# Kernel tuning notes

Measured on AMD Instinct MI355X. Metric: run time of the kernel, lower is better.

The kernel has to match this reference:

```python
import jax, jax.numpy as jnp
import numpy as np

NEG = 0.01  # leaky relu negative_slope
N = 4096    # neurons in this (relu) layer == rows of prev linear W
M = 4096    # inputs to prev linear layer


def setup_inputs() -> dict:
    key = jax.random.key(0)
    k1, k2, k3, k4, k5, k6, k7 = jax.random.split(key, 7)
    center = jax.random.normal(k1, (N,), dtype=jnp.float32)
    radius = jax.random.uniform(k2, (N,), dtype=jnp.float32)
    lowerBound = center - radius
    upperBound = center + radius
    alpha = jax.random.uniform(k3, (N,), minval=NEG, maxval=1.0, dtype=jnp.float32)
    W = jax.random.normal(k4, (N, M), dtype=jnp.float32) / np.float32(np.sqrt(M))
    b = jax.random.normal(k5, (N,), dtype=jnp.float32) * 0.1
    c0 = jax.random.normal(k6, (M,), dtype=jnp.float32)
    r0 = jax.random.uniform(k7, (M,), dtype=jnp.float32)
    return dict(lowerBound=lowerBound, upperBound=upperBound, alpha=alpha,
                W=W, b=b, l0=c0 - r0, u0=c0 + r0)


def reference(lowerBound, upperBound, alpha, W, b, l0, u0):
    ns = jnp.float32(NEG)
    # per-neuron slope/bias bounds (elementwise, exactly as the torch code)
    lw = jnp.full_like(lowerBound, ns)
    uw = jnp.full_like(upperBound, ns)
    ub_bias = jnp.zeros_like(upperBound)
    lb_bias = jnp.zeros_like(lowerBound)
    positive = lowerBound > 0
    lw = jnp.where(positive, 1.0, lw)
    uw = jnp.where(positive, 1.0, uw)
    crossing = (lowerBound < 0) & (upperBound > 0)
    slope = jnp.where(crossing,
                      (upperBound - ns * lowerBound) / (upperBound - lowerBound),
                      0.0)
    uw = jnp.where(crossing, slope, uw)
    ub_bias = jnp.where(crossing, (ns - slope) * lowerBound, ub_bias)
    a = jnp.clip(alpha, ns, 1.0)  # alpha.data.clamp_
    lw = jnp.where(crossing, a, lw)

    # faithful: materialize dense diagonal relational weight matrices [N,N]
    D_l = jnp.diag(lw)
    D_u = jnp.diag(uw)

    # prev (linear) backsubstitution: sign-split + four matmuls + bias accumulation
    Dup, Dun = jnp.maximum(D_u, 0.0), jnp.minimum(D_u, 0.0)
    Dlp, Dln = jnp.maximum(D_l, 0.0), jnp.minimum(D_l, 0.0)
    ub_bias = ub_bias + Dup @ b + Dun @ b   # linear layer: upper bias == lower bias == b
    lb_bias = lb_bias + Dlp @ b + Dln @ b
    Wu = Dup @ W + Dun @ W                  # [N,M]
    Wl = Dlp @ W + Dln @ W

    # input-layer concretization against the input box [l0, u0]
    upper = jnp.maximum(Wu, 0.0) @ u0 + jnp.minimum(Wu, 0.0) @ l0 + ub_bias
    lower = jnp.maximum(Wl, 0.0) @ l0 + jnp.minimum(Wl, 0.0) @ u0 + lb_bias
    return jnp.stack([lower, upper])  # [2, N]
```

## Files before the change

### kernel.cpp

```cpp
#include <hip/hip_runtime.h>

#define NN 4096
#define MM 4096
#define NEG 0.01f

__global__ __launch_bounds__(256, 4) void abstract_leaky_relu_kernel(
    const float* __restrict__ lbnd,
    const float* __restrict__ ubnd,
    const float* __restrict__ alpha,
    const float* __restrict__ W,
    const float* __restrict__ b,
    const float* __restrict__ l0,
    const float* __restrict__ u0,
    float* __restrict__ out)
{
    __shared__ float s_c[MM];
    __shared__ float s_r[MM];

    for (int j = threadIdx.x * 4; j < MM; j += 256 * 4) {
        const float4 l = *(const float4*)(l0 + j);
        const float4 u = *(const float4*)(u0 + j);
        *(float4*)(s_c + j) = make_float4(0.5f*(l.x+u.x), 0.5f*(l.y+u.y),
                                          0.5f*(l.z+u.z), 0.5f*(l.w+u.w));
        *(float4*)(s_r + j) = make_float4(0.5f*(u.x-l.x), 0.5f*(u.y-l.y),
                                          0.5f*(u.z-l.z), 0.5f*(u.w-l.w));
    }
    __syncthreads();

    const int wave = threadIdx.x >> 6;
    const int lane = threadIdx.x & 63;
    const int row  = (blockIdx.x << 2) + wave;

    const float* __restrict__ Wr = W + (size_t)row * MM;
    const int base = lane * 4;

    float s1a = 0.f, s1b = 0.f, s2a = 0.f, s2b = 0.f;

    #pragma unroll
    for (int t = 0; t < 16; ++t) {
        const int j = base + t * 256;
        const float4 w = *(const float4*)(Wr + j);
        const float4 c = *(const float4*)(s_c + j);
        const float4 r = *(const float4*)(s_r + j);
        if (t & 1) {
            s1b += w.x * c.x + w.y * c.y + w.z * c.z + w.w * c.w;
            s2b += fabsf(w.x) * r.x + fabsf(w.y) * r.y +
                   fabsf(w.z) * r.z + fabsf(w.w) * r.w;
        } else {
            s1a += w.x * c.x + w.y * c.y + w.z * c.z + w.w * c.w;
            s2a += fabsf(w.x) * r.x + fabsf(w.y) * r.y +
                   fabsf(w.z) * r.z + fabsf(w.w) * r.w;
        }
    }

    float s1 = s1a + s1b;
    float s2 = s2a + s2b;

    #pragma unroll
    for (int off = 32; off > 0; off >>= 1) {
        s1 += __shfl_down(s1, off);
        s2 += __shfl_down(s2, off);
    }

    if (lane == 0) {
        const float L = lbnd[row];
        const float U = ubnd[row];
        const float A = alpha[row];
        const float B = b[row];

        float lw = NEG, uw = NEG, ub_bias = 0.0f;
        if (L > 0.0f) {
            lw = 1.0f; uw = 1.0f;
        } else if (L < 0.0f && U > 0.0f) {
            const float slope = (U - NEG * L) / (U - L);
            uw = slope;
            ub_bias = (NEG - slope) * L;
            lw = fminf(fmaxf(A, NEG), 1.0f);
        }

        const float Pu = s1 + s2;
        const float Pl = s1 - s2;
        out[row]      = lw * (Pl + B);
        out[NN + row] = uw * (Pu + B) + ub_bias;
    }
}

extern "C" void kernel_launch(void* const* d_in, const int* in_sizes, int n_in,
                              void* d_out, int out_size, void* d_ws, size_t ws_size,
                              hipStream_t stream) {
    const float* lbnd  = (const float*)d_in[0];
    const float* ubnd  = (const float*)d_in[1];
    const float* alpha = (const float*)d_in[2];
    const float* W     = (const float*)d_in[3];
    const float* b     = (const float*)d_in[4];
    const float* l0    = (const float*)d_in[5];
    const float* u0    = (const float*)d_in[6];
    float* out = (float*)d_out;

    abstract_leaky_relu_kernel<<<NN / 4, 256, 0, stream>>>(
        lbnd, ubnd, alpha, W, b, l0, u0, out);
}
```

Baseline: 103.6 us.

## Drop shared-memory staging, split rows across two waves, nontemporal W loads

Result: slower. 113.0 us (+9.1%).

```diff
diff --git a/kernel.cpp b/kernel.cpp
--- a/kernel.cpp
+++ b/kernel.cpp
@@ -3,6 +3,8 @@
 #define NN 4096
 #define MM 4096
 #define NEG 0.01f
+
+typedef float floatx4 __attribute__((ext_vector_type(4)));
 
 __global__ __launch_bounds__(256, 4) void abstract_leaky_relu_kernel(
     const float* __restrict__ lbnd,
@@ -14,42 +16,40 @@
     const float* __restrict__ u0,
     float* __restrict__ out)
 {
-    __shared__ float s_c[MM];
-    __shared__ float s_r[MM];
-
-    for (int j = threadIdx.x * 4; j < MM; j += 256 * 4) {
-        const float4 l = *(const float4*)(l0 + j);
-        const float4 u = *(const float4*)(u0 + j);
-        *(float4*)(s_c + j) = make_float4(0.5f*(l.x+u.x), 0.5f*(l.y+u.y),
-                                          0.5f*(l.z+u.z), 0.5f*(l.w+u.w));
-        *(float4*)(s_r + j) = make_float4(0.5f*(u.x-l.x), 0.5f*(u.y-l.y),
-                                          0.5f*(u.z-l.z), 0.5f*(u.w-l.w));
-    }
-    __syncthreads();
+    __shared__ float pS1[4];
+    __shared__ float pS2[4];
 
     const int wave = threadIdx.x >> 6;
     const int lane = threadIdx.x & 63;
-    const int row  = (blockIdx.x << 2) + wave;
+    const int row  = (blockIdx.x << 1) + (wave >> 1);
+    const int half = wave & 1;
 
     const float* __restrict__ Wr = W + (size_t)row * MM;
-    const int base = lane * 4;
+    const int base = (half << 11) + (lane << 2);
 
     float s1a = 0.f, s1b = 0.f, s2a = 0.f, s2b = 0.f;
 
     #pragma unroll
-    for (int t = 0; t < 16; ++t) {
+    for (int t = 0; t < 8; ++t) {
         const int j = base + t * 256;
-        const float4 w = *(const float4*)(Wr + j);
-        const float4 c = *(const float4*)(s_c + j);
-        const float4 r = *(const float4*)(s_r + j);
+        const floatx4 w = __builtin_nontemporal_load(
+            reinterpret_cast<const floatx4*>(Wr + j));
+        const float4 l = *reinterpret_cast<const float4*>(l0 + j);
+        const float4 u = *reinterpret_cast<const float4*>(u0 + j);
+
+        const float cx = l.x + u.x, cy = l.y + u.y;
+        const float cz = l.z + u.z, cw = l.w + u.w;
+        const float rx = u.x - l.x, ry = u.y - l.y;
+        const float rz = u.z - l.z, rw = u.w - l.w;
+
         if (t & 1) {
-            s1b += w.x * c.x + w.y * c.y + w.z * c.z + w.w * c.w;
-            s2b += fabsf(w.x) * r.x + fabsf(w.y) * r.y +
-                   fabsf(w.z) * r.z + fabsf(w.w) * r.w;
+            s1b += w.x * cx + w.y * cy + w.z * cz + w.w * cw;
+            s2b += fabsf(w.x) * rx + fabsf(w.y) * ry +
+                   fabsf(w.z) * rz + fabsf(w.w) * rw;
         } else {
-            s1a += w.x * c.x + w.y * c.y + w.z * c.z + w.w * c.w;
-            s2a += fabsf(w.x) * r.x + fabsf(w.y) * r.y +
-                   fabsf(w.z) * r.z + fabsf(w.w) * r.w;
+            s1a += w.x * cx + w.y * cy + w.z * cz + w.w * cw;
+            s2a += fabsf(w.x) * rx + fabsf(w.y) * ry +
+                   fabsf(w.z) * rz + fabsf(w.w) * rw;
         }
     }
 
@@ -62,11 +62,22 @@
         s2 += __shfl_down(s2, off);
     }
 
-    if (lane == 0) {
-        const float L = lbnd[row];
-        const float U = ubnd[row];
-        const float A = alpha[row];
-        const float B = b[row];
+    if (lane == 0) { pS1[wave] = s1; pS2[wave] = s2; }
+    __syncthreads();
+
+    if (threadIdx.x < 2) {
+        const int r    = threadIdx.x;
+        const int row2 = (blockIdx.x << 1) + r;
+
+        const float S1 = pS1[2 * r] + pS1[2 * r + 1];
+        const float S2 = pS2[2 * r] + pS2[2 * r + 1];
+        const float Pu = 0.5f * (S1 + S2);
+        const float Pl = 0.5f * (S1 - S2);
+
+        const float L = lbnd[row2];
+        const float U = ubnd[row2];
+        const float A = alpha[row2];
+        const float B = b[row2];
 
         float lw = NEG, uw = NEG, ub_bias = 0.0f;
         if (L > 0.0f) {
@@ -78,10 +89,8 @@
             lw = fminf(fmaxf(A, NEG), 1.0f);
         }
 
-        const float Pu = s1 + s2;
-        const float Pl = s1 - s2;
-        out[row]      = lw * (Pl + B);
-        out[NN + row] = uw * (Pu + B) + ub_bias;
+        out[row2]      = lw * (Pl + B);
+        out[NN + row2] = uw * (Pu + B) + ub_bias;
     }
 }
 
@@ -97,6 +106,6 @@
     const float* u0    = (const float*)d_in[6];
     float* out = (float*)d_out;
 
-    abstract_leaky_relu_kernel<<<NN / 4, 256, 0, stream>>>(
+    abstract_leaky_relu_kernel<<<NN / 2, 256, 0, stream>>>(
         lbnd, ubnd, alpha, W, b, l0, u0, out);
 }
```

## Split columns across waves and keep input-box center/radius in registers

Applied to the files above, without the earlier changes.

After: 107.5 us. +3.8%, slower.

```diff
diff --git a/kernel.cpp b/kernel.cpp
--- a/kernel.cpp
+++ b/kernel.cpp
@@ -3,6 +3,7 @@
 #define NN 4096
 #define MM 4096
 #define NEG 0.01f
+#define ROWS 4
 
 __global__ __launch_bounds__(256, 4) void abstract_leaky_relu_kernel(
     const float* __restrict__ lbnd,
@@ -14,55 +15,67 @@
     const float* __restrict__ u0,
     float* __restrict__ out)
 {
-    __shared__ float s_c[MM];
-    __shared__ float s_r[MM];
+    const int wave = threadIdx.x >> 6;
+    const int lane = threadIdx.x & 63;
+    const int row0 = blockIdx.x * ROWS;
+    const int base = (wave << 10) + (lane << 2);
 
-    for (int j = threadIdx.x * 4; j < MM; j += 256 * 4) {
-        const float4 l = *(const float4*)(l0 + j);
-        const float4 u = *(const float4*)(u0 + j);
-        *(float4*)(s_c + j) = make_float4(0.5f*(l.x+u.x), 0.5f*(l.y+u.y),
-                                          0.5f*(l.z+u.z), 0.5f*(l.w+u.w));
-        *(float4*)(s_r + j) = make_float4(0.5f*(u.x-l.x), 0.5f*(u.y-l.y),
-                                          0.5f*(u.z-l.z), 0.5f*(u.w-l.w));
+    float4 c[4], r[4];
+    #pragma unroll
+    for (int q = 0; q < 4; ++q) {
+        const int j = base + q * 256;
+        const float4 l = *reinterpret_cast<const float4*>(l0 + j);
+        const float4 u = *reinterpret_cast<const float4*>(u0 + j);
+        c[q] = make_float4(l.x + u.x, l.y + u.y, l.z + u.z, l.w + u.w);
+        r[q] = make_float4(u.x - l.x, u.y - l.y, u.z - l.z, u.w - l.w);
+    }
+
+    float s1[ROWS], s2[ROWS];
+    #pragma unroll
+    for (int rr = 0; rr < ROWS; ++rr) { s1[rr] = 0.f; s2[rr] = 0.f; }
+
+    #pragma unroll
+    for (int rr = 0; rr < ROWS; ++rr) {
+        const float* __restrict__ Wr = W + (size_t)(row0 + rr) * MM + base;
+        #pragma unroll
+        for (int q = 0; q < 4; ++q) {
+            const float4 w = *reinterpret_cast<const float4*>(Wr + q * 256);
+            s1[rr] += w.x * c[q].x + w.y * c[q].y +
+                      w.z * c[q].z + w.w * c[q].w;
+            s2[rr] += fabsf(w.x) * r[q].x + fabsf(w.y) * r[q].y +
+                      fabsf(w.z) * r[q].z + fabsf(w.w) * r[q].w;
+        }
+    }
+
+    #pragma unroll
+    for (int off = 32; off > 0; off >>= 1) {
+        #pragma unroll
+        for (int rr = 0; rr < ROWS; ++rr) {
+            s1[rr] += __shfl_down(s1[rr], off);
+            s2[rr] += __shfl_down(s2[rr], off);
+        }
+    }
+
+    __shared__ float pS1[4][ROWS];
+    __shared__ float pS2[4][ROWS];
+    if (lane == 0) {
+        #pragma unroll
+        for (int rr = 0; rr < ROWS; ++rr) {
+            pS1[wave][rr] = s1[rr];
+            pS2[wave][rr] = s2[rr];
+        }
     }
     __syncthreads();
 
-    const int wave = threadIdx.x >> 6;
-    const int lane = threadIdx.x & 63;
-    const int row  = (blockIdx.x << 2) + wave;
+    if (threadIdx.x < ROWS) {
+        const int rr  = threadIdx.x;
+        const int row = row0 + rr;
 
-    const float* __restrict__ Wr = W + (size_t)row * MM;
-    const int base = lane * 4;
+        const float S1 = pS1[0][rr] + pS1[1][rr] + pS1[2][rr] + pS1[3][rr];
+        const float S2 = pS2[0][rr] + pS2[1][rr] + pS2[2][rr] + pS2[3][rr];
+        const float Pu = 0.5f * (S1 + S2);
+        const float Pl = 0.5f * (S1 - S2);
 
-    float s1a = 0.f, s1b = 0.f, s2a = 0.f, s2b = 0.f;
-
-    #pragma unroll
-    for (int t = 0; t < 16; ++t) {
-        const int j = base + t * 256;
-        const float4 w = *(const float4*)(Wr + j);
-        const float4 c = *(const float4*)(s_c + j);
-        const float4 r = *(const float4*)(s_r + j);
-        if (t & 1) {
-            s1b += w.x * c.x + w.y * c.y + w.z * c.z + w.w * c.w;
-            s2b += fabsf(w.x) * r.x + fabsf(w.y) * r.y +
-                   fabsf(w.z) * r.z + fabsf(w.w) * r.w;
-        } else {
-            s1a += w.x * c.x + w.y * c.y + w.z * c.z + w.w * c.w;
-            s2a += fabsf(w.x) * r.x + fabsf(w.y) * r.y +
-                   fabsf(w.z) * r.z + fabsf(w.w) * r.w;
-        }
-    }
-
-    float s1 = s1a + s1b;
-    float s2 = s2a + s2b;
-
-    #pragma unroll
-    for (int off = 32; off > 0; off >>= 1) {
-        s1 += __shfl_down(s1, off);
-        s2 += __shfl_down(s2, off);
-    }
-
-    if (lane == 0) {
         const float L = lbnd[row];
         const float U = ubnd[row];
         const float A = alpha[row];
@@ -78,8 +91,6 @@
             lw = fminf(fmaxf(A, NEG), 1.0f);
         }
 
-        const float Pu = s1 + s2;
-        const float Pl = s1 - s2;
         out[row]      = lw * (Pl + B);
         out[NN + row] = uw * (Pu + B) + ub_bias;
     }
@@ -97,6 +108,6 @@
     const float* u0    = (const float*)d_in[6];
     float* out = (float*)d_out;
 
-    abstract_leaky_relu_kernel<<<NN / 4, 256, 0, stream>>>(
+    abstract_leaky_relu_kernel<<<NN / ROWS, 256, 0, stream>>>(
         lbnd, ubnd, alpha, W, b, l0, u0, out);
 }
```
